# Kernel tuning notes

Measured on AMD Instinct MI355X. Metric: run time of the kernel, lower is better.

## Reference

```python
import jax, jax.numpy as jnp
import numpy as np

N_PARTICLES = 3_000_000
N_CVS = 30_000
N_MODELS = 8
FEATS = [64, 64, 64, 64]
E0, E1 = 2.0, 3.0
LN_EPS = 1e-5


def _dihedral(p):
    # p: [4,3] -> scalar dihedral angle (standard atan2 formulation)
    b1 = p[1] - p[0]
    b2 = p[2] - p[1]
    b3 = p[3] - p[2]
    n1 = jnp.cross(b1, b2)
    n2 = jnp.cross(b2, b3)
    m1 = jnp.cross(n1, b2 / jnp.linalg.norm(b2))
    return jnp.arctan2(jnp.dot(m1, n2), jnp.dot(n1, n2))


def _ensemble_energy(cvs, gamma, beta, Ws, bs):
    # cvs: [n_cvs] -> energy per model: [n_models]
    x = jnp.concatenate([jnp.cos(cvs), jnp.sin(cvs)])  # [2*n_cvs]
    mu = jnp.mean(x)
    var = jnp.mean((x - mu) ** 2)
    x = (x - mu) / jnp.sqrt(var + LN_EPS) * gamma + beta  # LayerNorm
    h = x[None, None, :]  # [1,1,2n] broadcasts against [M,2n,f]
    for i in range(len(Ws) - 1):
        h = jax.nn.relu(jnp.matmul(h, Ws[i]) + bs[i])  # [M,1,f]
    h = jnp.matmul(h, Ws[-1]) + bs[-1]  # [M,1,1]
    return h[:, 0, 0]  # [M]  (squeeze(-1) then batch dim 1)


def _uncertainty_weight(model_div):
    iswitch = (E1 - model_div) / (E1 - E0)
    fl = jnp.floor(iswitch)
    smooth = 0.5 * (1.0 + jnp.cos(jnp.pi * (1.0 - iswitch)))
    # heaviside(floor(iswitch), smooth): 1 if floor>0, smooth if floor==0, 0 if floor<0
    return jnp.where(fl > 0, 1.0, jnp.where(fl < 0, 0.0, smooth)).astype(model_div.dtype)


def setup_inputs() -> dict:
    key = jax.random.key(0)
    ks = jax.random.split(key, 16)
    positions = jax.random.normal(ks[0], (N_PARTICLES, 3), jnp.float32) * 3.0
    boxvectors = jnp.diag(jnp.full((3,), 10.0, dtype=jnp.float32))
    colvar_idx = jax.random.randint(ks[1], (N_CVS, 4), 0, N_PARTICLES)
    dims = [2 * N_CVS] + FEATS + [1]
    inp = {"positions": positions, "boxvectors": boxvectors, "colvar_idx": colvar_idx,
           "gamma": jnp.ones((2 * N_CVS,), jnp.float32),
           "beta": jnp.zeros((2 * N_CVS,), jnp.float32)}
    for i in range(5):
        bound = 1.0 / np.sqrt(dims[i])  # kaiming_uniform-like bound
        inp[f"W{i}"] = jax.random.uniform(ks[2 + i], (N_MODELS, dims[i], dims[i + 1]),
                                           jnp.float32, -bound, bound)
        inp[f"b{i}"] = jnp.zeros((N_MODELS, 1, dims[i + 1]), jnp.float32)
    return inp


def reference(positions, boxvectors, colvar_idx, gamma, beta,
              W0, b0, W1, b1, W2, b2, W3, b3, W4, b4):
    Ws = [W0, W1, W2, W3, W4]
    bs = [b0, b1, b2, b3, b4]
    boxsize = jnp.diag(boxvectors)  # [3]
    pos = positions - jnp.floor(positions / boxsize) * boxsize  # PBC wrap
    quads = pos[colvar_idx.reshape(-1)].reshape(-1, 4, 3)  # [n_cvs,4,3]
    cvs, dcvs_dx = jax.vmap(jax.value_and_grad(_dihedral))(quads)  # [n],[n,4,3]

    efn = lambda c: _ensemble_energy(c, gamma, beta, Ws, bs)  # [M]
    energy = efn(cvs)  # [M]
    mean_forces = -jax.jacrev(efn)(cvs)  # [M, n_cvs]: grad of -energy[m] wrt cvs

    model_div = jnp.sqrt(jnp.mean(jnp.var(mean_forces, axis=0, ddof=1)))
    sigma = _uncertainty_weight(model_div)
    mf = jnp.mean(mean_forces, axis=0)  # [n_cvs]
    contrib = (mf[:, None, None] * dcvs_dx).reshape(-1, 3)  # [n_cvs*4,3]
    forces = jnp.zeros_like(pos).at[colvar_idx.reshape(-1)].add(contrib)
    return energy.mean() * sigma, forces * sigma
```

## Files before the change

### kernel.cpp

```cpp
#include <hip/hip_runtime.h>
#include <math.h>

#define NCV   30000
#define NX    60000
#define NM    8
#define LN_EPSF 1e-5f
#define NFORCE 9000000

#define NB_CV 512
#define JB    59
#define NBX   235
#define NB_MF 118

#define WS_XRAW   0
#define WS_DCV    60000
#define WS_G      420000
#define WS_MF     900000
#define WS_LNP    930000
#define WS_Z0P    931024
#define WS_DZ0    961232
#define WS_E      961744
#define WS_SGP    961752
#define WS_SGXP   963632
#define WS_VARSUM 965512
#define WS_TICKET 965513
#define WS_SIGMA  965514

struct F3 { float x, y, z; };
__device__ __forceinline__ F3 f3sub(F3 a, F3 b){ return {a.x-b.x, a.y-b.y, a.z-b.z}; }
__device__ __forceinline__ F3 f3add(F3 a, F3 b){ return {a.x+b.x, a.y+b.y, a.z+b.z}; }
__device__ __forceinline__ F3 f3scale(F3 a, float s){ return {a.x*s, a.y*s, a.z*s}; }
__device__ __forceinline__ float f3dot(F3 a, F3 b){ return a.x*b.x + a.y*b.y + a.z*b.z; }
__device__ __forceinline__ F3 f3cross(F3 a, F3 b){
  return { a.y*b.z - a.z*b.y, a.z*b.x - a.x*b.z, a.x*b.y - a.y*b.x };
}

__device__ __forceinline__ void compute_mu_inv(const float* __restrict__ ws, float* out2, int tid) {
  if (tid < 64) {
    float a = 0.f, b = 0.f;
    #pragma unroll 4
    for (int k = tid; k < NB_CV; k += 64) { a += ws[WS_LNP + k]; b += ws[WS_LNP + NB_CV + k]; }
    #pragma unroll
    for (int o = 1; o < 64; o <<= 1) { a += __shfl_xor(a, o); b += __shfl_xor(b, o); }
    if (tid == 0) {
      float mu  = a * (1.f / NX);
      float var = b * (1.f / NX) - mu * mu;
      out2[0] = mu;
      out2[1] = 1.f / sqrtf(var + LN_EPSF);
    }
  }
}

__global__ void k_cv(const float* __restrict__ pos, const float* __restrict__ box,
                     const int* __restrict__ idx, float* __restrict__ ws,
                     float* __restrict__ out) {
  int tid = threadIdx.x;
  int gtid = blockIdx.x * 256 + tid;

  {
    float4 z4 = {0.f, 0.f, 0.f, 0.f};
    float4* fz = (float4*)(out + 4);
    const int NF4 = (NFORCE - 4) / 4;
    for (int i = gtid; i < NF4; i += NB_CV * 256) fz[i] = z4;
    if (gtid == 0) {
      out[1] = 0.f; out[2] = 0.f; out[3] = 0.f; out[NFORCE] = 0.f;
      ws[WS_VARSUM] = 0.f; ws[WS_TICKET] = 0.f;
    }
  }

  float cx = 0.f, cx2 = 0.f;
  int i = gtid;
  if (i < NCV) {
    float bx = box[0], by = box[4], bz = box[8];
    F3 p[4];
    #pragma unroll
    for (int a = 0; a < 4; a++) {
      int pi = idx[i*4 + a];
      float X = pos[(size_t)pi*3 + 0];
      float Y = pos[(size_t)pi*3 + 1];
      float Z = pos[(size_t)pi*3 + 2];
      X -= floorf(X / bx) * bx;
      Y -= floorf(Y / by) * by;
      Z -= floorf(Z / bz) * bz;
      p[a] = {X, Y, Z};
    }
    F3 b1 = f3sub(p[1], p[0]);
    F3 b2 = f3sub(p[2], p[1]);
    F3 b3 = f3sub(p[3], p[2]);
    F3 n1 = f3cross(b1, b2);
    F3 n2 = f3cross(b2, b3);
    float L = sqrtf(f3dot(b2, b2));
    F3 u = f3scale(b2, 1.f / L);
    F3 m1 = f3cross(n1, u);
    float yv = f3dot(m1, n2);
    float xv = f3dot(n1, n2);
    float h = sqrtf(xv*xv + yv*yv);
    float cphi = xv / h;
    float sphi = yv / h;

    float invd = 1.f / (h*h);
    float dX = -yv * invd;
    float dY =  xv * invd;
    F3 dn1 = f3scale(n2, dX);
    F3 dn2 = f3scale(n1, dX);
    F3 dm1 = f3scale(n2, dY);
    dn2 = f3add(dn2, f3scale(m1, dY));
    dn1 = f3add(dn1, f3cross(u, dm1));
    F3 du = f3cross(dm1, n1);
    float ud = f3dot(u, du);
    F3 db2 = f3scale(f3sub(du, f3scale(u, ud)), 1.f / L);
    db2 = f3add(db2, f3cross(b3, dn2));
    F3 db3 = f3cross(dn2, b2);
    F3 db1 = f3cross(b2, dn1);
    db2 = f3add(db2, f3cross(dn1, b1));

    F3 g0 = f3scale(db1, -1.f);
    F3 g1 = f3sub(db1, db2);
    F3 g2 = f3sub(db2, db3);
    F3 g3 = db3;

    ws[WS_XRAW + i]       = cphi;
    ws[WS_XRAW + NCV + i] = sphi;
    float* dc = ws + WS_DCV + (size_t)i * 12;
    dc[0] = g0.x; dc[1]  = g0.y; dc[2]  = g0.z;
    dc[3] = g1.x; dc[4]  = g1.y; dc[5]  = g1.z;
    dc[6] = g2.x; dc[7]  = g2.y; dc[8]  = g2.z;
    dc[9] = g3.x; dc[10] = g3.y; dc[11] = g3.z;

    cx  = cphi + sphi;
    cx2 = cphi*cphi + sphi*sphi;
  }

  #pragma unroll
  for (int o = 1; o < 64; o <<= 1) { cx += __shfl_xor(cx, o); cx2 += __shfl_xor(cx2, o); }
  __shared__ float sa[4], sb[4];
  int w = tid >> 6, l = tid & 63;
  if (l == 0) { sa[w] = cx; sb[w] = cx2; }
  __syncthreads();
  if (tid == 0) {
    ws[WS_LNP + blockIdx.x]         = sa[0] + sa[1] + sa[2] + sa[3];
    ws[WS_LNP + NB_CV + blockIdx.x] = sb[0] + sb[1] + sb[2] + sb[3];
  }
}

__global__ void k_z0(const float4* __restrict__ W0, const float* __restrict__ gamma,
                     const float* __restrict__ beta, float* __restrict__ ws) {
  __shared__ float stats[2];
  __shared__ float yl[1024];
  __shared__ float red[4][16][4];
  int tid = threadIdx.x;
  int jb = blockIdx.x, m = blockIdx.y;
  int j0 = jb * 1024;
  int jcount = min(1024, NX - j0);

  compute_mu_inv(ws, stats, tid);
  __syncthreads();
  float mu = stats[0], inv = stats[1];
  for (int jj = tid; jj < 1024; jj += 256) {
    int gj = j0 + jj;
    yl[jj] = (gj < NX) ? ((ws[WS_XRAW + gj] - mu) * inv * gamma[gj] + beta[gj]) : 0.f;
  }
  __syncthreads();

  int k4 = tid & 15;
  int r  = tid >> 4;
  const float4* Wm = W0 + (size_t)m * NX * 16;
  float4 acc = {0.f, 0.f, 0.f, 0.f};
  #pragma unroll 4
  for (int j = r; j < jcount; j += 16) {
    float y = yl[j];
    float4 wv = Wm[(size_t)(j0 + j) * 16 + k4];
    acc.x += y * wv.x; acc.y += y * wv.y; acc.z += y * wv.z; acc.w += y * wv.w;
  }
  #pragma unroll
  for (int o = 16; o <= 32; o <<= 1) {
    acc.x += __shfl_xor(acc.x, o); acc.y += __shfl_xor(acc.y, o);
    acc.z += __shfl_xor(acc.z, o); acc.w += __shfl_xor(acc.w, o);
  }
  int w = tid >> 6, l = tid & 63;
  if (l < 16) {
    red[w][l][0] = acc.x; red[w][l][1] = acc.y; red[w][l][2] = acc.z; red[w][l][3] = acc.w;
  }
  __syncthreads();
  if (tid < 64) {
    int kk4 = tid & 15, c = tid >> 4;
    float v = red[0][kk4][c] + red[1][kk4][c] + red[2][kk4][c] + red[3][kk4][c];
    ws[WS_Z0P + ((size_t)m * JB + jb) * 64 + kk4 * 4 + c] = v;
  }
}

__global__ void k_mlp(const float* __restrict__ ws_ro, const float* __restrict__ b0,
                      const float* __restrict__ W1, const float* __restrict__ b1,
                      const float* __restrict__ W2, const float* __restrict__ b2,
                      const float* __restrict__ W3, const float* __restrict__ b3,
                      const float* __restrict__ W4, const float* __restrict__ b4,
                      float* __restrict__ ws) {
  int m = blockIdx.x, k = threadIdx.x;
  __shared__ float h0[64], h1[64], h2[64], d3[64], d2[64], d1[64];
  const float* W1m = W1 + m * 4096;
  const float* W2m = W2 + m * 4096;
  const float* W3m = W3 + m * 4096;

  float a0 = b0[m*64 + k];
  #pragma unroll 4
  for (int jb = 0; jb < JB; jb++) a0 += ws_ro[WS_Z0P + ((size_t)m * JB + jb) * 64 + k];
  h0[k] = fmaxf(a0, 0.f);
  __syncthreads();
  float a1 = b1[m*64 + k];
  #pragma unroll 8
  for (int t = 0; t < 64; t++) a1 += h0[t] * W1m[t*64 + k];
  h1[k] = fmaxf(a1, 0.f);
  __syncthreads();
  float a2 = b2[m*64 + k];
  #pragma unroll 8
  for (int t = 0; t < 64; t++) a2 += h1[t] * W2m[t*64 + k];
  h2[k] = fmaxf(a2, 0.f);
  __syncthreads();
  float a3 = b3[m*64 + k];
  #pragma unroll 8
  for (int t = 0; t < 64; t++) a3 += h2[t] * W3m[t*64 + k];
  float h3 = fmaxf(a3, 0.f);

  float w4 = W4[m*64 + k];
  float e = h3 * w4;
  #pragma unroll
  for (int o = 1; o < 64; o <<= 1) e += __shfl_xor(e, o);
  if (k == 0) ws[WS_E + m] = e + b4[m];

  float dz3 = (a3 > 0.f) ? w4 : 0.f;
  d3[k] = dz3;
  __syncthreads();
  float dh2 = 0.f;
  #pragma unroll 8
  for (int t = 0; t < 64; t++) dh2 += W3m[k*64 + t] * d3[t];
  float dz2 = (a2 > 0.f) ? dh2 : 0.f;
  d2[k] = dz2;
  __syncthreads();
  float dh1 = 0.f;
  #pragma unroll 8
  for (int t = 0; t < 64; t++) dh1 += W2m[k*64 + t] * d2[t];
  float dz1 = (a1 > 0.f) ? dh1 : 0.f;
  d1[k] = dz1;
  __syncthreads();
  float dh0 = 0.f;
  #pragma unroll 8
  for (int t = 0; t < 64; t++) dh0 += W1m[k*64 + t] * d1[t];
  ws[WS_DZ0 + m*64 + k] = (a0 > 0.f) ? dh0 : 0.f;
}

__global__ void k_bwdx(const float4* __restrict__ W0, const float* __restrict__ gamma,
                       float* __restrict__ ws) {
  __shared__ float stats[2];
  __shared__ float dz[64];
  __shared__ float sa[4], sb[4];
  int tid = threadIdx.x;
  int m = blockIdx.y, blk = blockIdx.x;

  compute_mu_inv(ws, stats, tid);
  if (tid >= 64 && tid < 128) dz[tid - 64] = ws[WS_DZ0 + m*64 + (tid - 64)];
  __syncthreads();
  float mu = stats[0], inv = stats[1];

  int c = tid & 15;
  int g = tid >> 4;
  const float4* dz4 = (const float4*)dz;
  float4 d4 = dz4[c];

  float sg = 0.f, sgx = 0.f;
  #pragma unroll 2
  for (int it = 0; it < 16; it++) {
    int j = blk * 256 + it * 16 + g;
    if (j < NX) {
      float4 wv = W0[((size_t)m * NX + j) * 16 + c];
      float dot = wv.x*d4.x + wv.y*d4.y + wv.z*d4.z + wv.w*d4.w;
      #pragma unroll
      for (int o = 1; o < 16; o <<= 1) dot += __shfl_xor(dot, o);
      if (c == 0) {
        float gg = dot * gamma[j];
        ws[WS_G + (size_t)m * NX + j] = gg;
        float xh = (ws[WS_XRAW + j] - mu) * inv;
        sg += gg; sgx += gg * xh;
      }
    }
  }
  #pragma unroll
  for (int o = 1; o < 64; o <<= 1) { sg += __shfl_xor(sg, o); sgx += __shfl_xor(sgx, o); }
  int w = tid >> 6, l = tid & 63;
  if (l == 0) { sa[w] = sg; sb[w] = sgx; }
  __syncthreads();
  if (tid == 0) {
    ws[WS_SGP  + m * NBX + blk] = sa[0] + sa[1] + sa[2] + sa[3];
    ws[WS_SGXP + m * NBX + blk] = sb[0] + sb[1] + sb[2] + sb[3];
  }
}

__global__ void k_mf(float* __restrict__ ws, float* __restrict__ out) {
  __shared__ float stats[2];
  __shared__ float sSg[NM], sSgx[NM];
  __shared__ float sv[4];
  int tid = threadIdx.x;
  int w = tid >> 6, l = tid & 63;

  compute_mu_inv(ws, stats, tid);
  for (int m = w; m < NM; m += 4) {
    float a = 0.f, b = 0.f;
    #pragma unroll 2
    for (int bb = l; bb < NBX; bb += 64) { a += ws[WS_SGP + m*NBX + bb]; b += ws[WS_SGXP + m*NBX + bb]; }
    #pragma unroll
    for (int o = 1; o < 64; o <<= 1) { a += __shfl_xor(a, o); b += __shfl_xor(b, o); }
    if (l == 0) { sSg[m] = a * (1.f / NX); sSgx[m] = b * (1.f / NX); }
  }
  __syncthreads();
  float mu = stats[0], inv = stats[1];

  int i = blockIdx.x * 256 + tid;
  float v = 0.f;
  if (i < NCV) {
    float cph = ws[WS_XRAW + i], sph = ws[WS_XRAW + NCV + i];
    float xc = (cph - mu) * inv, xs = (sph - mu) * inv;
    float f[NM];
    float fm = 0.f;
    #pragma unroll
    for (int m = 0; m < NM; m++) {
      float gc = ws[WS_G + (size_t)m * NX + i];
      float gs = ws[WS_G + (size_t)m * NX + NCV + i];
      float dxc = inv * (gc - sSg[m] - xc * sSgx[m]);
      float dxs = inv * (gs - sSg[m] - xs * sSgx[m]);
      float dE = dxc * (-sph) + dxs * cph;
      f[m] = -dE;
      fm += f[m];
    }
    fm *= (1.f / NM);
    ws[WS_MF + i] = fm;
    float acc = 0.f;
    #pragma unroll
    for (int m = 0; m < NM; m++) { float d = f[m] - fm; acc += d * d; }
    v = acc * (1.f / (NM - 1));
  }
  #pragma unroll
  for (int o = 1; o < 64; o <<= 1) v += __shfl_xor(v, o);
  if (l == 0) sv[w] = v;
  __syncthreads();
  if (tid == 0) {
    atomicAdd(&ws[WS_VARSUM], sv[0] + sv[1] + sv[2] + sv[3]);
    __threadfence();
    unsigned int* tick = (unsigned int*)&ws[WS_TICKET];
    unsigned int old = atomicAdd(tick, 1u);
    if (old == NB_MF - 1) {
      __threadfence();
      float tot = atomicAdd(&ws[WS_VARSUM], 0.0f);
      float md = sqrtf(tot * (1.f / NCV));
      float isw = (3.0f - md) / (3.0f - 2.0f);
      float fl = floorf(isw);
      float smooth = 0.5f * (1.f + cosf(3.14159265358979323846f * (1.f - isw)));
      float sigma = (fl > 0.f) ? 1.f : ((fl < 0.f) ? 0.f : smooth);
      float em = 0.f;
      #pragma unroll
      for (int m = 0; m < NM; m++) em += ws[WS_E + m];
      em *= (1.f / NM);
      out[0] = em * sigma;
      ws[WS_SIGMA] = sigma;
    }
  }
}

__global__ void k_scatter(const int* __restrict__ idx, const float* __restrict__ ws,
                          float* __restrict__ forces) {
  int t = blockIdx.x * blockDim.x + threadIdx.x;
  if (t >= NCV * 12) return;
  int i = t / 12, r = t - i * 12;
  int a = r / 3, d = r - a * 3;
  float sigma = ws[WS_SIGMA];
  float contrib = ws[WS_MF + i] * ws[WS_DCV + (size_t)i * 12 + r] * sigma;
  atomicAdd(&forces[(size_t)idx[i*4 + a] * 3 + d], contrib);
}

extern "C" void kernel_launch(void* const* d_in, const int* in_sizes, int n_in,
                              void* d_out, int out_size, void* d_ws, size_t ws_size,
                              hipStream_t stream) {
  const float* pos   = (const float*)d_in[0];
  const float* box   = (const float*)d_in[1];
  const int*   idx   = (const int*)  d_in[2];
  const float* gamma = (const float*)d_in[3];
  const float* beta  = (const float*)d_in[4];
  const float* W0 = (const float*)d_in[5];
  const float* b0 = (const float*)d_in[6];
  const float* W1 = (const float*)d_in[7];
  const float* b1 = (const float*)d_in[8];
  const float* W2 = (const float*)d_in[9];
  const float* b2 = (const float*)d_in[10];
  const float* W3 = (const float*)d_in[11];
  const float* b3 = (const float*)d_in[12];
  const float* W4 = (const float*)d_in[13];
  const float* b4 = (const float*)d_in[14];
  float* ws  = (float*)d_ws;
  float* out = (float*)d_out;

  k_cv<<<NB_CV, 256, 0, stream>>>(pos, box, idx, ws, out);
  k_z0<<<dim3(JB, NM), 256, 0, stream>>>((const float4*)W0, gamma, beta, ws);
  k_mlp<<<NM, 64, 0, stream>>>(ws, b0, W1, b1, W2, b2, W3, b3, W4, b4, ws);
  k_bwdx<<<dim3(NBX, NM), 256, 0, stream>>>((const float4*)W0, gamma, ws);
  k_mf<<<NB_MF, 256, 0, stream>>>(ws, out);
  k_scatter<<<(NCV * 12 + 255) / 256, 256, 0, stream>>>(idx, ws, out + 1);
}
```

Measured before the change: 95.22 us.

## Fuse force scatter into mean-force kernel, move zeroing, widen MLP block

Removes the separate scatter kernel. After the mean-force kernel's last-block ticket computes sigma, it publishes sigma through an agent-scope release flag that every block spin-waits on, and each thread then does its 12 atomic force adds directly. The mean-force workspace buffer goes away. Output zeroing moves from the CV kernel to the W0 matvec kernel, which keeps the CV kernel lighter and still finishes before the scatter. The MLP kernel now uses 256 threads with shared-memory weight copies and a 4-way split reduction. The spin-wait relies on all 118 blocks being co-resident, which is a deadlock risk if they are not.

Result: slower. 100.7 us (+5.7%).

```diff
diff --git a/kernel.cpp b/kernel.cpp
--- a/kernel.cpp
+++ b/kernel.cpp
@@ -15,16 +15,16 @@
 #define WS_XRAW   0
 #define WS_DCV    60000
 #define WS_G      420000
-#define WS_MF     900000
-#define WS_LNP    930000
-#define WS_Z0P    931024
-#define WS_DZ0    961232
-#define WS_E      961744
-#define WS_SGP    961752
-#define WS_SGXP   963632
-#define WS_VARSUM 965512
-#define WS_TICKET 965513
-#define WS_SIGMA  965514
+#define WS_LNP    900000
+#define WS_Z0P    901024
+#define WS_DZ0    931232
+#define WS_E      931744
+#define WS_SGP    931752
+#define WS_SGXP   933632
+#define WS_VARSUM 935512
+#define WS_TICKET 935513
+#define WS_SIGMA  935514
+#define WS_FLAG   935515
 
 struct F3 { float x, y, z; };
 __device__ __forceinline__ F3 f3sub(F3 a, F3 b){ return {a.x-b.x, a.y-b.y, a.z-b.z}; }
@@ -52,30 +52,25 @@
 }
 
 __global__ void k_cv(const float* __restrict__ pos, const float* __restrict__ box,
-                     const int* __restrict__ idx, float* __restrict__ ws,
-                     float* __restrict__ out) {
+                     const int* __restrict__ idx, float* __restrict__ ws) {
   int tid = threadIdx.x;
   int gtid = blockIdx.x * 256 + tid;
-
-  {
-    float4 z4 = {0.f, 0.f, 0.f, 0.f};
-    float4* fz = (float4*)(out + 4);
-    const int NF4 = (NFORCE - 4) / 4;
-    for (int i = gtid; i < NF4; i += NB_CV * 256) fz[i] = z4;
-    if (gtid == 0) {
-      out[1] = 0.f; out[2] = 0.f; out[3] = 0.f; out[NFORCE] = 0.f;
-      ws[WS_VARSUM] = 0.f; ws[WS_TICKET] = 0.f;
-    }
+  if (gtid == 0) {
+    ws[WS_VARSUM] = 0.f;
+    ((unsigned int*)ws)[WS_TICKET] = 0u;
+    ((unsigned int*)ws)[WS_FLAG]   = 0u;
   }
 
   float cx = 0.f, cx2 = 0.f;
   int i = gtid;
   if (i < NCV) {
     float bx = box[0], by = box[4], bz = box[8];
+    int4 q4 = *(const int4*)(idx + i*4);
+    int pidx[4] = {q4.x, q4.y, q4.z, q4.w};
     F3 p[4];
     #pragma unroll
     for (int a = 0; a < 4; a++) {
-      int pi = idx[i*4 + a];
+      int pi = pidx[a];
       float X = pos[(size_t)pi*3 + 0];
       float Y = pos[(size_t)pi*3 + 1];
       float Z = pos[(size_t)pi*3 + 2];
@@ -144,7 +139,8 @@
 }
 
 __global__ void k_z0(const float4* __restrict__ W0, const float* __restrict__ gamma,
-                     const float* __restrict__ beta, float* __restrict__ ws) {
+                     const float* __restrict__ beta, float* __restrict__ ws,
+                     float* __restrict__ out) {
   __shared__ float stats[2];
   __shared__ float yl[1024];
   __shared__ float red[4][16][4];
@@ -152,6 +148,15 @@
   int jb = blockIdx.x, m = blockIdx.y;
   int j0 = jb * 1024;
   int jcount = min(1024, NX - j0);
+
+  {
+    int gtid = (m * JB + jb) * 256 + tid;
+    float4 z4 = {0.f, 0.f, 0.f, 0.f};
+    float4* fz = (float4*)(out + 4);
+    const int NF4 = (NFORCE - 4) / 4;
+    for (int i = gtid; i < NF4; i += JB * NM * 256) fz[i] = z4;
+    if (gtid == 0) { out[1] = 0.f; out[2] = 0.f; out[3] = 0.f; out[NFORCE] = 0.f; }
+  }
 
   compute_mu_inv(ws, stats, tid);
   __syncthreads();
@@ -195,57 +200,82 @@
                       const float* __restrict__ W3, const float* __restrict__ b3,
                       const float* __restrict__ W4, const float* __restrict__ b4,
                       float* __restrict__ ws) {
-  int m = blockIdx.x, k = threadIdx.x;
-  __shared__ float h0[64], h1[64], h2[64], d3[64], d2[64], d1[64];
-  const float* W1m = W1 + m * 4096;
-  const float* W2m = W2 + m * 4096;
-  const float* W3m = W3 + m * 4096;
-
-  float a0 = b0[m*64 + k];
-  #pragma unroll 4
-  for (int jb = 0; jb < JB; jb++) a0 += ws_ro[WS_Z0P + ((size_t)m * JB + jb) * 64 + k];
-  h0[k] = fmaxf(a0, 0.f);
-  __syncthreads();
-  float a1 = b1[m*64 + k];
-  #pragma unroll 8
-  for (int t = 0; t < 64; t++) a1 += h0[t] * W1m[t*64 + k];
-  h1[k] = fmaxf(a1, 0.f);
-  __syncthreads();
-  float a2 = b2[m*64 + k];
-  #pragma unroll 8
-  for (int t = 0; t < 64; t++) a2 += h1[t] * W2m[t*64 + k];
-  h2[k] = fmaxf(a2, 0.f);
-  __syncthreads();
-  float a3 = b3[m*64 + k];
-  #pragma unroll 8
-  for (int t = 0; t < 64; t++) a3 += h2[t] * W3m[t*64 + k];
-  float h3 = fmaxf(a3, 0.f);
-
-  float w4 = W4[m*64 + k];
-  float e = h3 * w4;
-  #pragma unroll
-  for (int o = 1; o < 64; o <<= 1) e += __shfl_xor(e, o);
-  if (k == 0) ws[WS_E + m] = e + b4[m];
-
-  float dz3 = (a3 > 0.f) ? w4 : 0.f;
-  d3[k] = dz3;
-  __syncthreads();
-  float dh2 = 0.f;
-  #pragma unroll 8
-  for (int t = 0; t < 64; t++) dh2 += W3m[k*64 + t] * d3[t];
-  float dz2 = (a2 > 0.f) ? dh2 : 0.f;
-  d2[k] = dz2;
-  __syncthreads();
-  float dh1 = 0.f;
-  #pragma unroll 8
-  for (int t = 0; t < 64; t++) dh1 += W2m[k*64 + t] * d2[t];
-  float dz1 = (a1 > 0.f) ? dh1 : 0.f;
-  d1[k] = dz1;
-  __syncthreads();
-  float dh0 = 0.f;
-  #pragma unroll 8
-  for (int t = 0; t < 64; t++) dh0 += W1m[k*64 + t] * d1[t];
-  ws[WS_DZ0 + m*64 + k] = (a0 > 0.f) ? dh0 : 0.f;
+  int m = blockIdx.x;
+  int tid = threadIdx.x;
+  int k = tid & 63, q = tid >> 6;
+  __shared__ float Wl[3][64*65];
+  __shared__ float hs[4][64];
+  __shared__ float part[256];
+  __shared__ float ds[64];
+
+  const float* Wsrc0 = W1 + m*4096;
+  const float* Wsrc1 = W2 + m*4096;
+  const float* Wsrc2 = W3 + m*4096;
+  for (int e = tid; e < 4096; e += 256) {
+    int t = e >> 6, kk = e & 63;
+    Wl[0][t*65 + kk] = Wsrc0[e];
+    Wl[1][t*65 + kk] = Wsrc1[e];
+    Wl[2][t*65 + kk] = Wsrc2[e];
+  }
+
+  float p0 = 0.f;
+  for (int jb = q; jb < JB; jb += 4)
+    p0 += ws_ro[WS_Z0P + ((size_t)m * JB + jb) * 64 + k];
+  part[tid] = p0;
+  __syncthreads();
+  if (tid < 64) {
+    float a0 = b0[m*64 + k] + part[k] + part[64+k] + part[128+k] + part[192+k];
+    hs[0][k] = fmaxf(a0, 0.f);
+  }
+  __syncthreads();
+
+  #pragma unroll
+  for (int l = 0; l < 3; l++) {
+    float pp = 0.f;
+    #pragma unroll
+    for (int t0 = 0; t0 < 16; t0++) {
+      int t = q*16 + t0;
+      pp += hs[l][t] * Wl[l][t*65 + k];
+    }
+    part[tid] = pp;
+    __syncthreads();
+    if (tid < 64) {
+      const float* bl = (l==0) ? b1 : (l==1) ? b2 : b3;
+      float a = bl[m*64+k] + part[k] + part[64+k] + part[128+k] + part[192+k];
+      hs[l+1][k] = fmaxf(a, 0.f);
+    }
+    __syncthreads();
+  }
+
+  if (tid < 64) {
+    float w4k = W4[m*64 + k];
+    float e = hs[3][k] * w4k;
+    #pragma unroll
+    for (int o = 1; o < 64; o <<= 1) e += __shfl_xor(e, o);
+    if (k == 0) ws[WS_E + m] = e + b4[m];
+    ds[k] = (hs[3][k] > 0.f) ? w4k : 0.f;
+  }
+  __syncthreads();
+
+  #pragma unroll
+  for (int l = 2; l >= 0; l--) {
+    float pp = 0.f;
+    int t = k;
+    #pragma unroll
+    for (int k0 = 0; k0 < 16; k0++) {
+      int kk = q*16 + k0;
+      pp += Wl[l][t*65 + kk] * ds[kk];
+    }
+    part[tid] = pp;
+    __syncthreads();
+    if (tid < 64) {
+      float dh = part[k] + part[64+k] + part[128+k] + part[192+k];
+      float dz = (hs[l][k] > 0.f) ? dh : 0.f;
+      if (l == 0) ws[WS_DZ0 + m*64 + k] = dz;
+      else        ds[k] = dz;
+    }
+    __syncthreads();
+  }
 }
 
 __global__ void k_bwdx(const float4* __restrict__ W0, const float* __restrict__ gamma,
@@ -294,10 +324,12 @@
   }
 }
 
-__global__ void k_mf(float* __restrict__ ws, float* __restrict__ out) {
+__global__ void k_mf(const int* __restrict__ idx, float* __restrict__ ws,
+                     float* __restrict__ out) {
   __shared__ float stats[2];
   __shared__ float sSg[NM], sSgx[NM];
   __shared__ float sv[4];
+  __shared__ float ssig;
   int tid = threadIdx.x;
   int w = tid >> 6, l = tid & 63;
 
@@ -314,12 +346,11 @@
   float mu = stats[0], inv = stats[1];
 
   int i = blockIdx.x * 256 + tid;
-  float v = 0.f;
+  float v = 0.f, fm = 0.f;
   if (i < NCV) {
     float cph = ws[WS_XRAW + i], sph = ws[WS_XRAW + NCV + i];
     float xc = (cph - mu) * inv, xs = (sph - mu) * inv;
     float f[NM];
-    float fm = 0.f;
     #pragma unroll
     for (int m = 0; m < NM; m++) {
       float gc = ws[WS_G + (size_t)m * NX + i];
@@ -331,7 +362,6 @@
       fm += f[m];
     }
     fm *= (1.f / NM);
-    ws[WS_MF + i] = fm;
     float acc = 0.f;
     #pragma unroll
     for (int m = 0; m < NM; m++) { float d = f[m] - fm; acc += d * d; }
@@ -344,10 +374,9 @@
   if (tid == 0) {
     atomicAdd(&ws[WS_VARSUM], sv[0] + sv[1] + sv[2] + sv[3]);
     __threadfence();
-    unsigned int* tick = (unsigned int*)&ws[WS_TICKET];
+    unsigned int* tick = (unsigned int*)ws + WS_TICKET;
     unsigned int old = atomicAdd(tick, 1u);
     if (old == NB_MF - 1) {
-      __threadfence();
       float tot = atomicAdd(&ws[WS_VARSUM], 0.0f);
       float md = sqrtf(tot * (1.f / NCV));
       float isw = (3.0f - md) / (3.0f - 2.0f);
@@ -359,20 +388,39 @@
       for (int m = 0; m < NM; m++) em += ws[WS_E + m];
       em *= (1.f / NM);
       out[0] = em * sigma;
-      ws[WS_SIGMA] = sigma;
-    }
-  }
-}
-
-__global__ void k_scatter(const int* __restrict__ idx, const float* __restrict__ ws,
-                          float* __restrict__ forces) {
-  int t = blockIdx.x * blockDim.x + threadIdx.x;
-  if (t >= NCV * 12) return;
-  int i = t / 12, r = t - i * 12;
-  int a = r / 3, d = r - a * 3;
-  float sigma = ws[WS_SIGMA];
-  float contrib = ws[WS_MF + i] * ws[WS_DCV + (size_t)i * 12 + r] * sigma;
-  atomicAdd(&forces[(size_t)idx[i*4 + a] * 3 + d], contrib);
+      __hip_atomic_store(ws + WS_SIGMA, sigma, __ATOMIC_RELAXED, __HIP_MEMORY_SCOPE_AGENT);
+      __hip_atomic_store((unsigned int*)ws + WS_FLAG, 1u, __ATOMIC_RELEASE, __HIP_MEMORY_SCOPE_AGENT);
+    }
+    while (__hip_atomic_load((unsigned int*)ws + WS_FLAG, __ATOMIC_ACQUIRE,
+                             __HIP_MEMORY_SCOPE_AGENT) == 0u) {
+      __builtin_amdgcn_s_sleep(8);
+    }
+    ssig = __hip_atomic_load(ws + WS_SIGMA, __ATOMIC_RELAXED, __HIP_MEMORY_SCOPE_AGENT);
+  }
+  __syncthreads();
+  float sigma = ssig;
+
+  if (i < NCV) {
+    const float* dc = ws + WS_DCV + (size_t)i * 12;
+    float4 d0 = *(const float4*)(dc);
+    float4 d1 = *(const float4*)(dc + 4);
+    float4 d2 = *(const float4*)(dc + 8);
+    int4 q4 = *(const int4*)(idx + i*4);
+    float s = fm * sigma;
+    float* fp = out + 1;
+    atomicAdd(&fp[(size_t)q4.x*3 + 0], s*d0.x);
+    atomicAdd(&fp[(size_t)q4.x*3 + 1], s*d0.y);
+    atomicAdd(&fp[(size_t)q4.x*3 + 2], s*d0.z);
+    atomicAdd(&fp[(size_t)q4.y*3 + 0], s*d0.w);
+    atomicAdd(&fp[(size_t)q4.y*3 + 1], s*d1.x);
+    atomicAdd(&fp[(size_t)q4.y*3 + 2], s*d1.y);
+    atomicAdd(&fp[(size_t)q4.z*3 + 0], s*d1.z);
+    atomicAdd(&fp[(size_t)q4.z*3 + 1], s*d1.w);
+    atomicAdd(&fp[(size_t)q4.z*3 + 2], s*d2.x);
+    atomicAdd(&fp[(size_t)q4.w*3 + 0], s*d2.y);
+    atomicAdd(&fp[(size_t)q4.w*3 + 1], s*d2.z);
+    atomicAdd(&fp[(size_t)q4.w*3 + 2], s*d2.w);
+  }
 }
 
 extern "C" void kernel_launch(void* const* d_in, const int* in_sizes, int n_in,
@@ -396,10 +444,9 @@
   float* ws  = (float*)d_ws;
   float* out = (float*)d_out;
 
-  k_cv<<<NB_CV, 256, 0, stream>>>(pos, box, idx, ws, out);
-  k_z0<<<dim3(JB, NM), 256, 0, stream>>>((const float4*)W0, gamma, beta, ws);
-  k_mlp<<<NM, 64, 0, stream>>>(ws, b0, W1, b1, W2, b2, W3, b3, W4, b4, ws);
+  k_cv<<<NB_CV, 256, 0, stream>>>(pos, box, idx, ws);
+  k_z0<<<dim3(JB, NM), 256, 0, stream>>>((const float4*)W0, gamma, beta, ws, out);
+  k_mlp<<<NM, 256, 0, stream>>>(ws, b0, W1, b1, W2, b2, W3, b3, W4, b4, ws);
   k_bwdx<<<dim3(NBX, NM), 256, 0, stream>>>((const float4*)W0, gamma, ws);
-  k_mf<<<NB_MF, 256, 0, stream>>>(ws, out);
-  k_scatter<<<(NCV * 12 + 255) / 256, 256, 0, stream>>>(idx, ws, out + 1);
-}
+  k_mf<<<NB_MF, 256, 0, stream>>>(idx, ws, out);
+}
```
